# Kernel optimization log

Measured on AMD Instinct MI355X. Metric: run time of the kernel, lower is better.

The kernel has to match this reference:

```python
import jax, jax.numpy as jnp
import numpy as np

B, S, H, E = 64, 512, 1024, 768
UNIFORM_RATE = 0.1


def setup_inputs() -> dict:
    key = jax.random.key(0)
    k1, k2, k3, k4, k5 = jax.random.split(key, 5)
    text = jax.random.normal(k1, (B, S, H), dtype=jnp.float32)
    aspect = jax.random.normal(k2, (B, S, E), dtype=jnp.float32)
    w_text = jax.random.uniform(k3, (B, H, H), minval=-UNIFORM_RATE, maxval=UNIFORM_RATE, dtype=jnp.float32)
    w_aspect = jax.random.uniform(k4, (B, E, E), minval=-UNIFORM_RATE, maxval=UNIFORM_RATE, dtype=jnp.float32)
    w_combine = jax.random.uniform(k5, (B, 1, H + E), minval=-UNIFORM_RATE, maxval=UNIFORM_RATE, dtype=jnp.float32)
    return {"text": text, "aspect": aspect, "w_text": w_text, "w_aspect": w_aspect, "w_combine": w_combine}


def reference(text, aspect, w_text, w_aspect, w_combine):
    # text: [B,S,H] -> text_out: [B,H,S]; aspect: [B,S,E] -> [B,E,S]
    text_out = jnp.swapaxes(text, 1, 2)          # [B,H,S]
    aspect_out = jnp.swapaxes(aspect, 1, 2)      # [B,E,S]
    m_text = jnp.einsum('bhk,bks->bhs', w_text, text_out)       # [B,H,S]
    m_aspect = jnp.einsum('bef,bfs->bes', w_aspect, aspect_out)  # [B,E,S]
    combine = jnp.tanh(jnp.concatenate((m_text, m_aspect), axis=1))  # [B,H+E,S]
    scores = jnp.einsum('boc,bcs->bos', w_combine, combine)     # [B,1,S]
    weight = jax.nn.softmax(scores, axis=2)                     # softmax over seq dim
    # out = bmm(text_out [B,H,S], weight^T [B,S,1]) -> [B,H,1] -> permute -> [B,1,H]
    out = jnp.einsum('bhs,bos->boh', text_out, weight)          # [B,1,H]
    return (weight, out)
```

## Files before the change

### kernel.cpp

```cpp
#include <hip/hip_runtime.h>
#include <stdint.h>

#define Bn 64
#define Sn 512
#define Hn 1024
#define En 768
#define Cn (Hn + En)

typedef __bf16 bf16_t;
typedef bf16_t bf16x8 __attribute__((ext_vector_type(8)));
typedef float  f32x4  __attribute__((ext_vector_type(4)));
typedef unsigned int uint32;
typedef uint32 u32x4 __attribute__((ext_vector_type(4)));
typedef unsigned short ushort_t;

#define T_TEXT   33554432u
#define T_ASPECT 58720256u
#define T_WTEXT  125829120u
#define T_TOTAL  163577856u
#define WS_BF_BYTES ((size_t)T_TOTAL * 2)

__device__ __forceinline__ uint32 pack2_bf16(float a, float b) {
    uint32 ua = __float_as_uint(a) + 0x8000u;
    uint32 ub = __float_as_uint(b) + 0x8000u;
    return (ub & 0xFFFF0000u) | (ua >> 16);
}

__global__ __launch_bounds__(256)
void convert_kernel(const float* __restrict__ text, const float* __restrict__ aspect,
                    const float* __restrict__ w_text, const float* __restrict__ w_aspect,
                    ushort_t* __restrict__ dst)
{
    const size_t i = ((size_t)blockIdx.x * 256 + threadIdx.x) * 8;
    const float* src; size_t off;
    if (i < T_TEXT)        { src = text;     off = i; }
    else if (i < T_ASPECT) { src = aspect;   off = i - T_TEXT; }
    else if (i < T_WTEXT)  { src = w_text;   off = i - T_ASPECT; }
    else                   { src = w_aspect; off = i - T_WTEXT; }
    f32x4 a = *(const f32x4*)(src + off);
    f32x4 c = *(const f32x4*)(src + off + 4);
    u32x4 p = { pack2_bf16(a.x, a.y), pack2_bf16(a.z, a.w),
                pack2_bf16(c.x, c.y), pack2_bf16(c.z, c.w) };
    *(u32x4*)(dst + i) = p;
}


#define STAGE_A(SLOT, H, KT) do {                                                       \
    const ushort_t* _g = Ag + (size_t)((H) * 128) * K + (size_t)(KT) * 64;              \
    __builtin_amdgcn_global_load_lds(                                                   \
        (const __attribute__((address_space(1))) void*)_g,                              \
        (__attribute__((address_space(3))) void*)&As[SLOT][(H) * 128 + wid * 8][0],     \
        16, 0, 0);                                                                      \
    __builtin_amdgcn_global_load_lds(                                                   \
        (const __attribute__((address_space(1))) void*)(_g + (size_t)64 * K),           \
        (__attribute__((address_space(3))) void*)&As[SLOT][(H) * 128 + 64 + wid * 8][0],\
        16, 0, 0);                                                                      \
} while (0)

#define STAGE_B(SLOT, H, KT) do {                                                       \
    const ushort_t* _g = Bg + (size_t)((H) * 128) * K + (size_t)(KT) * 64;              \
    __builtin_amdgcn_global_load_lds(                                                   \
        (const __attribute__((address_space(1))) void*)_g,                              \
        (__attribute__((address_space(3))) void*)&Bs[SLOT][(H) * 128 + wid * 8][0],     \
        16, 0, 0);                                                                      \
    __builtin_amdgcn_global_load_lds(                                                   \
        (const __attribute__((address_space(1))) void*)(_g + (size_t)64 * K),           \
        (__attribute__((address_space(3))) void*)&Bs[SLOT][(H) * 128 + 64 + wid * 8][0],\
        16, 0, 0);                                                                      \
} while (0)

#define TAIL_NONE
#define TAIL_V4  asm volatile("s_waitcnt vmcnt(4)" ::: "memory");
#define TAIL_V4L if (nl) { asm volatile("s_waitcnt vmcnt(4)" ::: "memory"); }           \
                 else    { asm volatile("s_waitcnt vmcnt(0)" ::: "memory"); }

#define PHASE(SLOT, HQ, LQ, TAIL, ...) do {                                             \
    bf16x8 af[2][4], bv[2][2];                                                          \
    _Pragma("unroll")                                                                   \
    for (int ks = 0; ks < 2; ++ks) {                                                    \
        const int cc = ks ? c1 : c0;                                                    \
        _Pragma("unroll")                                                               \
        for (int mi = 0; mi < 4; ++mi)                                                  \
            af[ks][mi] = *(const bf16x8*)&As[SLOT][(HQ) * 128 + rowA0 + mi * 16][cc];   \
        _Pragma("unroll")                                                               \
        for (int nj = 0; nj < 2; ++nj)                                                  \
            bv[ks][nj] = *(const bf16x8*)&Bs[SLOT][(LQ) * 128 + rowB0 + nj * 16][cc];   \
    }                                                                                   \
    __VA_ARGS__;                                                                        \
    __builtin_amdgcn_sched_barrier(0);                                                  \
    __builtin_amdgcn_s_barrier();                                                       \
    asm volatile("s_waitcnt lgkmcnt(0)" ::: "memory");                                  \
    __builtin_amdgcn_sched_barrier(0);                                                  \
    __builtin_amdgcn_s_setprio(1);                                                      \
    _Pragma("unroll")                                                                   \
    for (int ks = 0; ks < 2; ++ks)                                                      \
        _Pragma("unroll")                                                               \
        for (int mi = 0; mi < 4; ++mi)                                                  \
            _Pragma("unroll")                                                           \
            for (int nj = 0; nj < 2; ++nj)                                              \
                acc[HQ][LQ][mi][nj] = __builtin_amdgcn_mfma_f32_16x16x32_bf16(          \
                    af[ks][mi], bv[ks][nj], acc[HQ][LQ][mi][nj], 0, 0, 0);              \
    __builtin_amdgcn_s_setprio(0);                                                      \
    TAIL                                                                                \
    __builtin_amdgcn_sched_barrier(0);                                                  \
    __builtin_amdgcn_s_barrier();                                                       \
} while (0)

__global__ __launch_bounds__(512, 2)
void scores_kernel(const ushort_t* __restrict__ text_bf,
                   const ushort_t* __restrict__ aspect_bf,
                   const ushort_t* __restrict__ wtext_bf,
                   const ushort_t* __restrict__ waspect_bf,
                   const float* __restrict__ w_combine,
                   float* __restrict__ scores)
{
    __shared__ __align__(16) ushort_t As[2][256][64];
    __shared__ __align__(16) ushort_t Bs[2][256][64];

    const int lin = blockIdx.x + 2 * (blockIdx.y + 7 * blockIdx.z);
    const int wg  = (lin & 7) * 112 + (lin >> 3);
    const int bx = wg % 2;
    const int by = (wg / 2) % 7;
    const int b  = wg / 14;

    const int m0 = by * 256;
    const int n0 = bx * 256;
    const bool is_text = (m0 < Hn);
    const int K  = is_text ? Hn : En;
    const int NI = K >> 7;
    const ushort_t* Amat = is_text ? (wtext_bf   + (size_t)b * Hn * Hn + (size_t)m0 * Hn)
                                   : (waspect_bf + (size_t)b * En * En + (size_t)(m0 - Hn) * En);
    const ushort_t* Bmat = is_text ? (text_bf   + (size_t)b * Sn * Hn + (size_t)n0 * Hn)
                                   : (aspect_bf + (size_t)b * Sn * En + (size_t)n0 * En);

    const int t = threadIdx.x;
    const int wid = t >> 6, lane = t & 63;
    const int r16 = lane & 15, q4 = lane >> 4;
    const int wr = wid >> 2, wc = wid & 3;
    const int rowA0 = wr * 64 + r16;
    const int rowB0 = wc * 32 + r16;
    const int c0 = ((0 + q4) ^ (r16 & 7)) * 8;
    const int c1 = ((4 + q4) ^ (r16 & 7)) * 8;

    const int srow = t >> 3;
    const int cg = (t & 7) ^ (srow & 7);
    const ushort_t* Ag = Amat + (size_t)srow * K + (size_t)cg * 8;
    const ushort_t* Bg = Bmat + (size_t)srow * K + (size_t)cg * 8;

    f32x4 acc[2][2][4][2];
    #pragma unroll
    for (int a0 = 0; a0 < 2; ++a0)
        #pragma unroll
        for (int a1 = 0; a1 < 2; ++a1)
            #pragma unroll
            for (int a2 = 0; a2 < 4; ++a2)
                #pragma unroll
                for (int a3 = 0; a3 < 2; ++a3)
                    acc[a0][a1][a2][a3] = (f32x4){0.f, 0.f, 0.f, 0.f};

    STAGE_A(0, 0, 0); STAGE_B(0, 0, 0);
    STAGE_A(0, 1, 0); STAGE_B(0, 1, 0);
    STAGE_A(1, 0, 1); STAGE_B(1, 0, 1);
    asm volatile("s_waitcnt vmcnt(4)" ::: "memory");
    __builtin_amdgcn_sched_barrier(0);
    __builtin_amdgcn_s_barrier();

    for (int it = 0; it < NI; ++it) {
        const int ktB = 2 * it + 1, kt2 = 2 * it + 2, kt3 = 2 * it + 3;
        const bool nl = (it + 1 < NI);
        PHASE(0, 0, 0, TAIL_NONE, STAGE_A(1, 1, ktB));
        PHASE(0, 0, 1, TAIL_NONE, STAGE_B(1, 1, ktB));
        PHASE(0, 1, 0, TAIL_NONE, if (nl) STAGE_A(0, 0, kt2));
        PHASE(0, 1, 1, TAIL_V4L,  if (nl) STAGE_B(0, 0, kt2));
        PHASE(1, 0, 0, TAIL_NONE, if (nl) STAGE_A(0, 1, kt2));
        PHASE(1, 0, 1, TAIL_NONE, if (nl) STAGE_B(0, 1, kt2));
        PHASE(1, 1, 0, TAIL_NONE, if (nl) STAGE_A(1, 0, kt3));
        PHASE(1, 1, 1, TAIL_V4,   if (nl) STAGE_B(1, 0, kt3));
    }

    float* partf = (float*)&As[0][0][0];
    float* wcs   = (float*)&Bs[0][0][0];
    if (t < 256) wcs[t] = w_combine[(size_t)b * Cn + m0 + t];
    __syncthreads();

    #pragma unroll
    for (int lq = 0; lq < 2; ++lq)
        #pragma unroll
        for (int nj = 0; nj < 2; ++nj) {
            float s = 0.f;
            #pragma unroll
            for (int hq = 0; hq < 2; ++hq)
                #pragma unroll
                for (int mi = 0; mi < 4; ++mi)
                    #pragma unroll
                    for (int r = 0; r < 4; ++r)
                        s += tanhf(acc[hq][lq][mi][nj][r])
                             * wcs[hq * 128 + wr * 64 + mi * 16 + q4 * 4 + r];
            s += __shfl_xor(s, 16, 64);
            s += __shfl_xor(s, 32, 64);
            if (q4 == 0) partf[(wid * 4 + lq * 2 + nj) * 16 + r16] = s;
        }
    __syncthreads();
    if (t < 256) {
        const int lq = t >> 7, wcq = (t >> 5) & 3, nj = (t >> 4) & 1, rr = t & 15;
        const float tot = partf[(wcq * 4 + lq * 2 + nj) * 16 + rr]
                        + partf[((4 + wcq) * 4 + lq * 2 + nj) * 16 + rr];
        atomicAdd(&scores[(size_t)b * Sn + n0 + t], tot);
    }
}

__global__ __launch_bounds__(256)
void softmax_kernel(const float* __restrict__ scores, float* __restrict__ weight)
{
    __shared__ float red[4];
    const int b = blockIdx.x, t = threadIdx.x;
    const int lane = t & 63, wid = t >> 6;
    const float v0 = scores[(size_t)b * Sn + t];
    const float v1 = scores[(size_t)b * Sn + 256 + t];
    float m = fmaxf(v0, v1);
    #pragma unroll
    for (int off = 32; off >= 1; off >>= 1) m = fmaxf(m, __shfl_xor(m, off, 64));
    if (lane == 0) red[wid] = m;
    __syncthreads();
    const float M = fmaxf(fmaxf(red[0], red[1]), fmaxf(red[2], red[3]));
    __syncthreads();
    const float e0 = expf(v0 - M), e1 = expf(v1 - M);
    float s = e0 + e1;
    #pragma unroll
    for (int off = 32; off >= 1; off >>= 1) s += __shfl_xor(s, off, 64);
    if (lane == 0) red[wid] = s;
    __syncthreads();
    const float inv = 1.0f / (red[0] + red[1] + red[2] + red[3]);
    weight[(size_t)b * Sn + t]       = e0 * inv;
    weight[(size_t)b * Sn + 256 + t] = e1 * inv;
}

__global__ __launch_bounds__(256)
void out_kernel(const float* __restrict__ text, const float* __restrict__ weight,
                float* __restrict__ out)
{
    __shared__ float ws[Sn];
    const int b = blockIdx.y, hc = blockIdx.x;
    const int t = threadIdx.x;
    ws[t]       = weight[(size_t)b * Sn + t];
    ws[t + 256] = weight[(size_t)b * Sn + 256 + t];
    __syncthreads();
    const int h = hc * 256 + t;
    const float* tb = text + (size_t)b * Sn * Hn + h;
    float acc = 0.f;
    #pragma unroll 8
    for (int s = 0; s < Sn; ++s)
        acc += tb[(size_t)s * Hn] * ws[s];
    out[(size_t)b * Hn + h] = acc;
}

extern "C" void kernel_launch(void* const* d_in, const int* in_sizes, int n_in,
                              void* d_out, int out_size, void* d_ws, size_t ws_size,
                              hipStream_t stream)
{
    const float* text      = (const float*)d_in[0];
    const float* aspect    = (const float*)d_in[1];
    const float* w_text    = (const float*)d_in[2];
    const float* w_aspect  = (const float*)d_in[3];
    const float* w_combine = (const float*)d_in[4];

    float* outp   = (float*)d_out;
    float* weight = outp;
    float* outv   = outp + (size_t)Bn * Sn;

    ushort_t* bf   = (ushort_t*)d_ws;
    float* scores  = (float*)((char*)d_ws + WS_BF_BYTES);

    const ushort_t* text_bf    = bf;
    const ushort_t* aspect_bf  = bf + T_TEXT;
    const ushort_t* wtext_bf   = bf + T_ASPECT;
    const ushort_t* waspect_bf = bf + T_WTEXT;

    hipMemsetAsync(scores, 0, (size_t)Bn * Sn * sizeof(float), stream);
    convert_kernel<<<T_TOTAL / 8 / 256, 256, 0, stream>>>(text, aspect, w_text, w_aspect, bf);
    scores_kernel<<<dim3(2, 7, Bn), 512, 0, stream>>>(text_bf, aspect_bf, wtext_bf, waspect_bf,
                                                      w_combine, scores);
    softmax_kernel<<<Bn, 256, 0, stream>>>(scores, weight);
    out_kernel<<<dim3(4, Bn), 256, 0, stream>>>(text, weight, outv);
}
```

Measured before the change: 856.5 us.

## Merge GEMM phases into four per iteration and use grid-stride conversion

The GEMM main loop goes from eight phases per iteration to four, each computing both B halves against one A half. This halves the number of block barriers and reorders the global-to-LDS staging and vmcnt waits to match. The conversion kernel becomes a grid-stride loop over a fixed 2048 blocks instead of one block per chunk. The merged phases keep more B fragments live in registers, and the new staging order changes how much load latency is hidden.

Measured after the change: 873.6 us. 1.02x slower.

```diff
diff --git a/kernel.cpp b/kernel.cpp
--- a/kernel.cpp
+++ b/kernel.cpp
@@ -31,17 +31,19 @@
                     const float* __restrict__ w_text, const float* __restrict__ w_aspect,
                     ushort_t* __restrict__ dst)
 {
-    const size_t i = ((size_t)blockIdx.x * 256 + threadIdx.x) * 8;
-    const float* src; size_t off;
-    if (i < T_TEXT)        { src = text;     off = i; }
-    else if (i < T_ASPECT) { src = aspect;   off = i - T_TEXT; }
-    else if (i < T_WTEXT)  { src = w_text;   off = i - T_ASPECT; }
-    else                   { src = w_aspect; off = i - T_WTEXT; }
-    f32x4 a = *(const f32x4*)(src + off);
-    f32x4 c = *(const f32x4*)(src + off + 4);
-    u32x4 p = { pack2_bf16(a.x, a.y), pack2_bf16(a.z, a.w),
-                pack2_bf16(c.x, c.y), pack2_bf16(c.z, c.w) };
-    *(u32x4*)(dst + i) = p;
+    const size_t stride = (size_t)gridDim.x * 256 * 8;
+    for (size_t i = ((size_t)blockIdx.x * 256 + threadIdx.x) * 8; i < T_TOTAL; i += stride) {
+        const float* src; size_t off;
+        if (i < T_TEXT)        { src = text;     off = i; }
+        else if (i < T_ASPECT) { src = aspect;   off = i - T_TEXT; }
+        else if (i < T_WTEXT)  { src = w_text;   off = i - T_ASPECT; }
+        else                   { src = w_aspect; off = i - T_WTEXT; }
+        f32x4 a = *(const f32x4*)(src + off);
+        f32x4 c = *(const f32x4*)(src + off + 4);
+        u32x4 p = { pack2_bf16(a.x, a.y), pack2_bf16(a.z, a.w),
+                    pack2_bf16(c.x, c.y), pack2_bf16(c.z, c.w) };
+        *(u32x4*)(dst + i) = p;
+    }
 }
 
 
@@ -70,12 +72,12 @@
 } while (0)
 
 #define TAIL_NONE
-#define TAIL_V4  asm volatile("s_waitcnt vmcnt(4)" ::: "memory");
-#define TAIL_V4L if (nl) { asm volatile("s_waitcnt vmcnt(4)" ::: "memory"); }           \
+#define TAIL_V2L if (nl) { asm volatile("s_waitcnt vmcnt(2)" ::: "memory"); }           \
                  else    { asm volatile("s_waitcnt vmcnt(0)" ::: "memory"); }
-
-#define PHASE(SLOT, HQ, LQ, TAIL, ...) do {                                             \
-    bf16x8 af[2][4], bv[2][2];                                                          \
+#define TAIL_V2N if (nl) { asm volatile("s_waitcnt vmcnt(2)" ::: "memory"); }
+
+#define PHASE4(SLOT, HQ, TAIL, ...) do {                                                \
+    bf16x8 af[2][4], bv[2][2][2];                                                       \
     _Pragma("unroll")                                                                   \
     for (int ks = 0; ks < 2; ++ks) {                                                    \
         const int cc = ks ? c1 : c0;                                                    \
@@ -83,8 +85,10 @@
         for (int mi = 0; mi < 4; ++mi)                                                  \
             af[ks][mi] = *(const bf16x8*)&As[SLOT][(HQ) * 128 + rowA0 + mi * 16][cc];   \
         _Pragma("unroll")                                                               \
-        for (int nj = 0; nj < 2; ++nj)                                                  \
-            bv[ks][nj] = *(const bf16x8*)&Bs[SLOT][(LQ) * 128 + rowB0 + nj * 16][cc];   \
+        for (int lq = 0; lq < 2; ++lq)                                                  \
+            _Pragma("unroll")                                                           \
+            for (int nj = 0; nj < 2; ++nj)                                              \
+                bv[lq][ks][nj] = *(const bf16x8*)&Bs[SLOT][lq * 128 + rowB0 + nj * 16][cc]; \
     }                                                                                   \
     __VA_ARGS__;                                                                        \
     __builtin_amdgcn_sched_barrier(0);                                                  \
@@ -95,11 +99,13 @@
     _Pragma("unroll")                                                                   \
     for (int ks = 0; ks < 2; ++ks)                                                      \
         _Pragma("unroll")                                                               \
-        for (int mi = 0; mi < 4; ++mi)                                                  \
+        for (int lq = 0; lq < 2; ++lq)                                                  \
             _Pragma("unroll")                                                           \
-            for (int nj = 0; nj < 2; ++nj)                                              \
-                acc[HQ][LQ][mi][nj] = __builtin_amdgcn_mfma_f32_16x16x32_bf16(          \
-                    af[ks][mi], bv[ks][nj], acc[HQ][LQ][mi][nj], 0, 0, 0);              \
+            for (int mi = 0; mi < 4; ++mi)                                              \
+                _Pragma("unroll")                                                       \
+                for (int nj = 0; nj < 2; ++nj)                                          \
+                    acc[HQ][lq][mi][nj] = __builtin_amdgcn_mfma_f32_16x16x32_bf16(      \
+                        af[ks][mi], bv[lq][ks][nj], acc[HQ][lq][mi][nj], 0, 0, 0);      \
     __builtin_amdgcn_s_setprio(0);                                                      \
     TAIL                                                                                \
     __builtin_amdgcn_sched_barrier(0);                                                  \
@@ -158,24 +164,19 @@
                 for (int a3 = 0; a3 < 2; ++a3)
                     acc[a0][a1][a2][a3] = (f32x4){0.f, 0.f, 0.f, 0.f};
 
-    STAGE_A(0, 0, 0); STAGE_B(0, 0, 0);
-    STAGE_A(0, 1, 0); STAGE_B(0, 1, 0);
-    STAGE_A(1, 0, 1); STAGE_B(1, 0, 1);
-    asm volatile("s_waitcnt vmcnt(4)" ::: "memory");
+    STAGE_A(0, 0, 0); STAGE_A(0, 1, 0); STAGE_B(0, 0, 0); STAGE_B(0, 1, 0);
+    STAGE_A(1, 0, 1);
+    asm volatile("s_waitcnt vmcnt(2)" ::: "memory");
     __builtin_amdgcn_sched_barrier(0);
     __builtin_amdgcn_s_barrier();
 
     for (int it = 0; it < NI; ++it) {
-        const int ktB = 2 * it + 1, kt2 = 2 * it + 2, kt3 = 2 * it + 3;
+        const int kt1 = 2 * it + 1, kt2 = 2 * it + 2, kt3 = 2 * it + 3;
         const bool nl = (it + 1 < NI);
-        PHASE(0, 0, 0, TAIL_NONE, STAGE_A(1, 1, ktB));
-        PHASE(0, 0, 1, TAIL_NONE, STAGE_B(1, 1, ktB));
-        PHASE(0, 1, 0, TAIL_NONE, if (nl) STAGE_A(0, 0, kt2));
-        PHASE(0, 1, 1, TAIL_V4L,  if (nl) STAGE_B(0, 0, kt2));
-        PHASE(1, 0, 0, TAIL_NONE, if (nl) STAGE_A(0, 1, kt2));
-        PHASE(1, 0, 1, TAIL_NONE, if (nl) STAGE_B(0, 1, kt2));
-        PHASE(1, 1, 0, TAIL_NONE, if (nl) STAGE_A(1, 0, kt3));
-        PHASE(1, 1, 1, TAIL_V4,   if (nl) STAGE_B(1, 0, kt3));
+        PHASE4(0, 0, TAIL_NONE, STAGE_A(1, 1, kt1); STAGE_B(1, 0, kt1); STAGE_B(1, 1, kt1));
+        PHASE4(0, 1, TAIL_V2L,  if (nl) STAGE_A(0, 0, kt2));
+        PHASE4(1, 0, TAIL_NONE, if (nl) { STAGE_A(0, 1, kt2); STAGE_B(0, 0, kt2); STAGE_B(0, 1, kt2); });
+        PHASE4(1, 1, TAIL_V2N,  if (nl) STAGE_A(1, 0, kt3));
     }
 
     float* partf = (float*)&As[0][0][0];
@@ -277,7 +278,7 @@
     const ushort_t* waspect_bf = bf + T_WTEXT;
 
     hipMemsetAsync(scores, 0, (size_t)Bn * Sn * sizeof(float), stream);
-    convert_kernel<<<T_TOTAL / 8 / 256, 256, 0, stream>>>(text, aspect, w_text, w_aspect, bf);
+    convert_kernel<<<2048, 256, 0, stream>>>(text, aspect, w_text, w_aspect, bf);
     scores_kernel<<<dim3(2, 7, Bn), 512, 0, stream>>>(text_bf, aspect_bf, wtext_bf, waspect_bf,
                                                       w_combine, scores);
     softmax_kernel<<<Bn, 256, 0, stream>>>(scores, weight);
```
